# Performance work log

Hardware: AMD Instinct MI355X
Metric: run time of the kernel (lower is better)

Reference implementation:

```python
import jax, jax.numpy as jnp
import numpy as np

N_NODES = 100000
N_EDGES = 1600000


def setup_inputs() -> dict:
    key = jax.random.key(0)
    ks = jax.random.split(key, 6)
    x = jax.random.normal(ks[0], (N_NODES, 166), dtype=jnp.float32)
    edge_index = jax.random.randint(ks[1], (2, N_EDGES), 0, N_NODES, dtype=jnp.int64)
    s = 0.05
    return {
        "x": x,
        "edge_index": edge_index,
        "W1l": jax.random.normal(ks[2], (166, 128), dtype=jnp.float32) * s,
        "b1": jnp.zeros((128,), dtype=jnp.float32),
        "W1r": jax.random.normal(ks[3], (166, 128), dtype=jnp.float32) * s,
        "W2l": jax.random.normal(ks[4], (128, 2), dtype=jnp.float32) * s,
        "b2": jnp.zeros((2,), dtype=jnp.float32),
        "W2r": jax.random.normal(ks[5], (128, 2), dtype=jnp.float32) * s,
    }


def _sage_mean_agg(h, src, dst, n_nodes):
    # mean over incoming edges (PyG SAGEConv default aggr='mean');
    # nodes with no in-edges get zeros.
    summed = jax.ops.segment_sum(h[src], dst, num_segments=n_nodes)
    deg = jax.ops.segment_sum(jnp.ones_like(dst, dtype=h.dtype), dst,
                              num_segments=n_nodes)
    return summed / jnp.maximum(deg, 1.0)[:, None]


def reference(x, edge_index, W1l, b1, W1r, W2l, b2, W2r):
    src, dst = edge_index[0], edge_index[1]
    n = x.shape[0]
    # layer 1: out = lin_l(mean_agg(x)) + lin_r(x)
    agg1 = _sage_mean_agg(x, src, dst, n)
    h = agg1 @ W1l + b1 + x @ W1r
    h = jax.nn.relu(h)
    # dropout p=0.5 is identity in eval mode
    # layer 2
    agg2 = _sage_mean_agg(h, src, dst, n)
    out = agg2 @ W2l + b2 + h @ W2r
    return jax.nn.log_softmax(out, axis=1)
```

## Files before the change

### kernel.cpp

```cpp
#include <hip/hip_runtime.h>
#include <hip/hip_bf16.h>
#include <math.h>

#define N_NODES 100000
#define N_EDGES 1600000
#define FDIM 166
#define HDIM 128
#define KP 192
#define CAP 64
#define YTP 264
#define MBLK 64
#define XCHUNKS 42
#define XPITCH 672
#define TOTCH (MBLK * XCHUNKS)
#define NXCD 8
#define NODES_PER (N_NODES / NXCD)

typedef __attribute__((ext_vector_type(8))) short bf16x8;
typedef __attribute__((ext_vector_type(4))) float f32x4;

#define GLOAD_LDS16(g, l) __builtin_amdgcn_global_load_lds( \
    (const __attribute__((address_space(1))) unsigned int*)(g), \
    (__attribute__((address_space(3))) unsigned int*)(l), 16, 0, 0)

__device__ inline float bf2f(unsigned short s) {
    unsigned int u = ((unsigned int)s) << 16;
    float f; __builtin_memcpy(&f, &u, 4); return f;
}
__device__ inline float bflo(unsigned int u) {
    unsigned int v = u << 16;
    float f; __builtin_memcpy(&f, &v, 4); return f;
}
__device__ inline float bfhi(unsigned int u) {
    unsigned int v = u & 0xffff0000u;
    float f; __builtin_memcpy(&f, &v, 4); return f;
}
__device__ inline unsigned short f2bf(float f) {
    unsigned int u; __builtin_memcpy(&u, &f, 4);
    unsigned int r = u + 0x7fffu + ((u >> 16) & 1u);
    return (unsigned short)(r >> 16);
}
__device__ inline bf16x8 pack8(float4 a, float4 b) {
    union { bf16x8 v; __hip_bfloat162 h[4]; } u;
    u.h[0] = __float22bfloat162_rn(make_float2(a.x, a.y));
    u.h[1] = __float22bfloat162_rn(make_float2(a.z, a.w));
    u.h[2] = __float22bfloat162_rn(make_float2(b.x, b.y));
    u.h[3] = __float22bfloat162_rn(make_float2(b.z, b.w));
    return u.v;
}

__global__ __launch_bounds__(256) void k_fill(const int* __restrict__ ei,
                                              int* __restrict__ cnt,
                                              int* __restrict__ adj) {
    int xcd = blockIdx.x & (NXCD - 1);
    int grp = blockIdx.x >> 3;
    int lo = xcd * NODES_PER, hi = lo + NODES_PER;
    int stride = (gridDim.x >> 3) * 256;
    for (int e = grp * 256 + threadIdx.x; e < N_EDGES; e += stride) {
        int d = ei[N_EDGES + e];
        if (d >= lo && d < hi) {
            int s = ei[e];
            int slot = atomicAdd(&cnt[d], 1);
            if (slot < CAP) adj[d * CAP + slot] = s;
        }
    }
}

__global__ void k_prepw(const float* __restrict__ W1l, const float* __restrict__ W1r,
                        unsigned short* __restrict__ wt) {
    int idx = blockIdx.x * 256 + threadIdx.x;
    int c = idx / KP, k = idx - c * KP;
    float v = 0.f;
    if (k < FDIM)
        v = (c < HDIM) ? W1l[k * HDIM + c] : W1r[k * HDIM + (c - HDIM)];
    wt[idx] = f2bf(v);
}

__global__ __launch_bounds__(256) void k_gemm(
        const float* __restrict__ x, const unsigned short* __restrict__ wt,
        unsigned short* __restrict__ yl, unsigned short* __restrict__ yr) {
    __shared__ __align__(16) char sm[43264];
    int tid = threadIdx.x;
    int r0 = blockIdx.x * MBLK;
    int w = tid >> 6, lane = tid & 63;

    if (tid < 32) *(float*)(sm + TOTCH * 16 + tid * 4) = 0.f;

    {
        int wbase = w * 64;
        #pragma unroll
        for (int rd = 0; rd < 11; ++rd) {
            int base = rd * 256 + wbase;
            if (base < TOTCH) {
                int idx = base + lane;
                int row = idx / XCHUNKS, c = idx - row * XCHUNKS;
                int gr = r0 + row; if (gr > N_NODES - 1) gr = N_NODES - 1;
                const char* src = (const char*)x + (size_t)gr * (FDIM * 4) + c * 16;
                GLOAD_LDS16(src, sm + base * 16);
            }
        }
    }
    __syncthreads();

    int rbase = (w >> 1) * 32;
    int c0 = (w & 1) * 128;
    int l15 = lane & 15, g = lane >> 4;

    f32x4 acc[2][8];
    #pragma unroll
    for (int a = 0; a < 2; a++)
        #pragma unroll
        for (int b = 0; b < 8; b++) acc[a][b] = (f32x4){0.f, 0.f, 0.f, 0.f};

    const char* wb = (const char*)wt;
    int wlane = (c0 + l15) * (KP * 2) + 16 * g;
    int brow0 = (rbase + l15) * XPITCH + 32 * g;
    int brow1 = brow0 + 16 * XPITCH;

    bf16x8 ww[2][8];
    #pragma unroll
    for (int cf = 0; cf < 8; cf++)
        ww[0][cf] = *(const bf16x8*)(wb + wlane + cf * (16 * KP * 2));

    #pragma unroll
    for (int kk = 0; kk < 6; ++kk) {
        int cur = kk & 1, nxt = cur ^ 1;
        if (kk < 5) {
            #pragma unroll
            for (int cf = 0; cf < 8; cf++)
                ww[nxt][cf] = *(const bf16x8*)(wb + wlane + cf * (16 * KP * 2) + (kk + 1) * 64);
        }
        float4 p0 = *(const float4*)(sm + brow0 + kk * 128);
        float4 q0 = *(const float4*)(sm + brow0 + kk * 128 + 16);
        float4 p1 = *(const float4*)(sm + brow1 + kk * 128);
        float4 q1 = *(const float4*)(sm + brow1 + kk * 128 + 16);
        bf16x8 xb0 = pack8(p0, q0);
        bf16x8 xb1 = pack8(p1, q1);
        #pragma unroll
        for (int cf = 0; cf < 8; cf++) {
            acc[0][cf] = __builtin_amdgcn_mfma_f32_16x16x32_bf16(ww[cur][cf], xb0, acc[0][cf], 0, 0, 0);
            acc[1][cf] = __builtin_amdgcn_mfma_f32_16x16x32_bf16(ww[cur][cf], xb1, acc[1][cf], 0, 0, 0);
        }
    }
    __syncthreads();

    #pragma unroll
    for (int rf = 0; rf < 2; rf++) {
        int row = rbase + 16 * rf + l15;
        #pragma unroll
        for (int cf = 0; cf < 8; cf++) {
            int col = c0 + 16 * cf + 4 * g;
            ushort4 o;
            o.x = f2bf(acc[rf][cf][0]); o.y = f2bf(acc[rf][cf][1]);
            o.z = f2bf(acc[rf][cf][2]); o.w = f2bf(acc[rf][cf][3]);
            *(ushort4*)(sm + row * (YTP * 2) + col * 2) = o;
        }
    }
    __syncthreads();

    for (int it = 0; it < 8; ++it) {
        int n = tid + it * 256;
        int row = n >> 5, c16 = n & 31;
        uint4 v = *(const uint4*)(sm + row * (YTP * 2) + c16 * 16);
        int gr = r0 + row;
        if (gr < N_NODES) {
            unsigned short* dst = (c16 < 16) ? yl : yr;
            *(uint4*)((char*)dst + (size_t)gr * 256 + (size_t)(c16 & 15) * 16) = v;
        }
    }
}

__global__ __launch_bounds__(256) void k_agg1(
        const unsigned short* __restrict__ yl, const unsigned short* __restrict__ yr,
        const int* __restrict__ cnt, const int* __restrict__ adj,
        const float* __restrict__ b1,
        const float* __restrict__ W2l, const float* __restrict__ W2r,
        float* __restrict__ zw) {
    int w = threadIdx.x >> 6, lane = threadIdx.x & 63;
    int i = blockIdx.x * 4 + w;
    if (i >= N_NODES) return;
    int deg = cnt[i];
    int n = min(deg, CAP);
    int aidx = adj[i * CAP + lane];
    float a0 = 0.f, a1 = 0.f, p0 = 0.f, p1 = 0.f, q0 = 0.f, q1 = 0.f, r0 = 0.f, r1 = 0.f;
    int j = 0;
    for (; j + 4 <= n; j += 4) {
        int s0 = __shfl(aidx, j, 64);
        int s1 = __shfl(aidx, j + 1, 64);
        int s2 = __shfl(aidx, j + 2, 64);
        int s3 = __shfl(aidx, j + 3, 64);
        unsigned int u0 = *(const unsigned int*)&yl[(size_t)s0 * HDIM + lane * 2];
        unsigned int u1 = *(const unsigned int*)&yl[(size_t)s1 * HDIM + lane * 2];
        unsigned int u2 = *(const unsigned int*)&yl[(size_t)s2 * HDIM + lane * 2];
        unsigned int u3 = *(const unsigned int*)&yl[(size_t)s3 * HDIM + lane * 2];
        a0 += bflo(u0); a1 += bfhi(u0);
        p0 += bflo(u1); p1 += bfhi(u1);
        q0 += bflo(u2); q1 += bfhi(u2);
        r0 += bflo(u3); r1 += bfhi(u3);
    }
    for (; j < n; ++j) {
        int s = __shfl(aidx, j, 64);
        unsigned int u = *(const unsigned int*)&yl[(size_t)s * HDIM + lane * 2];
        a0 += bflo(u); a1 += bfhi(u);
    }
    a0 += p0 + q0 + r0;
    a1 += p1 + q1 + r1;
    float inv = 1.f / (float)max(deg, 1);
    unsigned int ur = *(const unsigned int*)&yr[(size_t)i * HDIM + lane * 2];
    float2 bb = *(const float2*)&b1[lane * 2];
    float h0 = fmaxf(a0 * inv + bflo(ur) + bb.x, 0.f);
    float h1 = fmaxf(a1 * inv + bfhi(ur) + bb.y, 0.f);
    float4 wl2 = *(const float4*)&W2l[lane * 4];
    float4 wr2 = *(const float4*)&W2r[lane * 4];
    float z0 = h0 * wl2.x + h1 * wl2.z;
    float z1 = h0 * wl2.y + h1 * wl2.w;
    float w0 = h0 * wr2.x + h1 * wr2.z;
    float w1 = h0 * wr2.y + h1 * wr2.w;
    #pragma unroll
    for (int m = 32; m; m >>= 1) {
        z0 += __shfl_xor(z0, m, 64); z1 += __shfl_xor(z1, m, 64);
        w0 += __shfl_xor(w0, m, 64); w1 += __shfl_xor(w1, m, 64);
    }
    if (lane == 0) {
        float4 o = {z0, z1, w0, w1};
        *(float4*)&zw[i * 4] = o;
    }
}

__global__ void k_out(const float* __restrict__ zw, const int* __restrict__ cnt,
                      const int* __restrict__ adj, const float* __restrict__ b2,
                      float* __restrict__ out) {
    int i = blockIdx.x * 256 + threadIdx.x;
    if (i >= N_NODES) return;
    int deg = cnt[i];
    int n = min(deg, CAP);
    float s0 = 0.f, s1 = 0.f;
    const int* arow = adj + i * CAP;
    for (int j = 0; j < n; j++) {
        int s = arow[j];
        float2 zz = *(const float2*)&zw[s * 4];
        s0 += zz.x; s1 += zz.y;
    }
    float inv = 1.f / (float)max(deg, 1);
    float p0 = s0 * inv + b2[0] + zw[i * 4 + 2];
    float p1 = s1 * inv + b2[1] + zw[i * 4 + 3];
    float mx = fmaxf(p0, p1);
    float lse = mx + logf(expf(p0 - mx) + expf(p1 - mx));
    out[i * 2 + 0] = p0 - lse;
    out[i * 2 + 1] = p1 - lse;
}

extern "C" void kernel_launch(void* const* d_in, const int* in_sizes, int n_in,
                              void* d_out, int out_size, void* d_ws, size_t ws_size,
                              hipStream_t stream) {
    const float* x   = (const float*)d_in[0];
    const int*   ei  = (const int*)d_in[1];
    const float* W1l = (const float*)d_in[2];
    const float* b1  = (const float*)d_in[3];
    const float* W1r = (const float*)d_in[4];
    const float* W2l = (const float*)d_in[5];
    const float* b2  = (const float*)d_in[6];
    const float* W2r = (const float*)d_in[7];
    float* out = (float*)d_out;

    char* ws = (char*)d_ws;
    size_t off = 0;
    auto alloc = [&](size_t bytes) {
        off = (off + 255) & ~(size_t)255;
        void* p = ws + off;
        off += bytes;
        return p;
    };
    int* cnt            = (int*)alloc((size_t)N_NODES * 4);
    int* adj            = (int*)alloc((size_t)N_NODES * CAP * 4);
    unsigned short* wt  = (unsigned short*)alloc((size_t)256 * KP * 2);
    unsigned short* yl  = (unsigned short*)alloc((size_t)N_NODES * HDIM * 2);
    unsigned short* yr  = (unsigned short*)alloc((size_t)N_NODES * HDIM * 2);
    float* zw           = (float*)alloc((size_t)N_NODES * 4 * 4);
    (void)ws_size; (void)in_sizes; (void)n_in; (void)out_size;

    hipMemsetAsync(cnt, 0, (size_t)N_NODES * 4, stream);
    k_fill<<<2048, 256, 0, stream>>>(ei, cnt, adj);
    k_prepw<<<(256 * KP) / 256, 256, 0, stream>>>(W1l, W1r, wt);
    k_gemm<<<(N_NODES + MBLK - 1) / MBLK, 256, 0, stream>>>(x, wt, yl, yr);
    k_agg1<<<(N_NODES + 3) / 4, 256, 0, stream>>>(yl, yr, cnt, adj, b1, W2l, W2r, zw);
    k_out<<<(N_NODES + 255) / 256, 256, 0, stream>>>(zw, cnt, adj, b2, out);
}
```

Baseline: 223.6 us.

## Fuse adjacency fill with layer-1 GEMM and fold memset into weight prep

Merges the edge-bucketing fill kernel into the GEMM kernel as extra interleaved blocks, so the atomic-heavy, latency-bound fill can overlap with the compute-bound GEMM on the same launch. The count memset is folded into the weight-prep kernel, cutting launches from four to two. Fill blocks keep their XCD affinity through the block-index interleave and now number 1024 instead of 2048. The trade-offs are that fill blocks reserve the GEMM's shared-memory footprint, and that per-block work is uneven across the grid.

```diff
diff --git a/kernel.cpp b/kernel.cpp
--- a/kernel.cpp
+++ b/kernel.cpp
@@ -15,6 +15,9 @@
 #define TOTCH (MBLK * XCHUNKS)
 #define NXCD 8
 #define NODES_PER (N_NODES / NXCD)
+#define FILLB 1024
+#define GEMMB ((N_NODES + MBLK - 1) / MBLK)
+#define TOTB (GEMMB + FILLB)
 
 typedef __attribute__((ext_vector_type(8))) short bf16x8;
 typedef __attribute__((ext_vector_type(4))) float f32x4;
@@ -49,39 +52,50 @@
     return u.v;
 }
 
-__global__ __launch_bounds__(256) void k_fill(const int* __restrict__ ei,
-                                              int* __restrict__ cnt,
-                                              int* __restrict__ adj) {
-    int xcd = blockIdx.x & (NXCD - 1);
-    int grp = blockIdx.x >> 3;
-    int lo = xcd * NODES_PER, hi = lo + NODES_PER;
-    int stride = (gridDim.x >> 3) * 256;
-    for (int e = grp * 256 + threadIdx.x; e < N_EDGES; e += stride) {
-        int d = ei[N_EDGES + e];
-        if (d >= lo && d < hi) {
-            int s = ei[e];
-            int slot = atomicAdd(&cnt[d], 1);
-            if (slot < CAP) adj[d * CAP + slot] = s;
-        }
-    }
-}
-
-__global__ void k_prepw(const float* __restrict__ W1l, const float* __restrict__ W1r,
-                        unsigned short* __restrict__ wt) {
+__global__ void k_pre(const float* __restrict__ W1l, const float* __restrict__ W1r,
+                      unsigned short* __restrict__ wt, int* __restrict__ cnt) {
     int idx = blockIdx.x * 256 + threadIdx.x;
-    int c = idx / KP, k = idx - c * KP;
-    float v = 0.f;
-    if (k < FDIM)
-        v = (c < HDIM) ? W1l[k * HDIM + c] : W1r[k * HDIM + (c - HDIM)];
-    wt[idx] = f2bf(v);
-}
-
-__global__ __launch_bounds__(256) void k_gemm(
+    if (blockIdx.x < 192) {
+        int c = idx / KP, k = idx - c * KP;
+        float v = 0.f;
+        if (k < FDIM)
+            v = (c < HDIM) ? W1l[k * HDIM + c] : W1r[k * HDIM + (c - HDIM)];
+        wt[idx] = f2bf(v);
+    } else {
+        int i = idx - 192 * 256;
+        if (i < N_NODES) cnt[i] = 0;
+    }
+}
+
+__global__ __launch_bounds__(256) void k_fused(
         const float* __restrict__ x, const unsigned short* __restrict__ wt,
-        unsigned short* __restrict__ yl, unsigned short* __restrict__ yr) {
+        unsigned short* __restrict__ yl, unsigned short* __restrict__ yr,
+        const int* __restrict__ ei, int* __restrict__ cnt, int* __restrict__ adj) {
     __shared__ __align__(16) char sm[43264];
+    int bid = blockIdx.x;
+    int id; bool isfill;
+    if (bid < 2 * FILLB) {
+        isfill = (bid >> 3) & 1;
+        id = ((bid >> 4) << 3) | (bid & 7);
+    } else { isfill = false; id = bid - FILLB; }
+
+    if (isfill) {
+        int xcd = bid & (NXCD - 1);
+        int lo = xcd * NODES_PER, hi = lo + NODES_PER;
+        int stride = (FILLB >> 3) * 256;
+        for (int e = (id >> 3) * 256 + threadIdx.x; e < N_EDGES; e += stride) {
+            int d = ei[N_EDGES + e];
+            if (d >= lo && d < hi) {
+                int s = ei[e];
+                int slot = atomicAdd(&cnt[d], 1);
+                if (slot < CAP) adj[d * CAP + slot] = s;
+            }
+        }
+        return;
+    }
+
     int tid = threadIdx.x;
-    int r0 = blockIdx.x * MBLK;
+    int r0 = id * MBLK;
     int w = tid >> 6, lane = tid & 63;
 
     if (tid < 32) *(float*)(sm + TOTCH * 16 + tid * 4) = 0.f;
@@ -279,10 +293,8 @@
     float* zw           = (float*)alloc((size_t)N_NODES * 4 * 4);
     (void)ws_size; (void)in_sizes; (void)n_in; (void)out_size;
 
-    hipMemsetAsync(cnt, 0, (size_t)N_NODES * 4, stream);
-    k_fill<<<2048, 256, 0, stream>>>(ei, cnt, adj);
-    k_prepw<<<(256 * KP) / 256, 256, 0, stream>>>(W1l, W1r, wt);
-    k_gemm<<<(N_NODES + MBLK - 1) / MBLK, 256, 0, stream>>>(x, wt, yl, yr);
+    k_pre<<<192 + (N_NODES + 255) / 256, 256, 0, stream>>>(W1l, W1r, wt, cnt);
+    k_fused<<<TOTB, 256, 0, stream>>>(x, wt, yl, yr, ei, cnt, adj);
     k_agg1<<<(N_NODES + 3) / 4, 256, 0, stream>>>(yl, yr, cnt, adj, b1, W2l, W2r, zw);
     k_out<<<(N_NODES + 255) / 256, 256, 0, stream>>>(zw, cnt, adj, b2, out);
 }
```

Result: slower. 249.1 us (+11.4%).
